# Kernel optimization log

Hardware: AMD Instinct MI355X
Metric: run time of the kernel (lower is better)

The kernel has to match this reference:

```python
import jax, jax.numpy as jnp
import numpy as np
from jax import lax

C = 384        # in_channels
K = 16         # number of frames selected (self.k)
SIGMA = 0.05   # perturbation sigma (forward arg, hardcoded)
NUM_SAMPLES = 500


def setup_inputs() -> dict:
    key = jax.random.key(0)
    ks = jax.random.split(key, 8)
    B, T, N = 16, 32, 196
    D = 2 * C  # PredictorLG embed_dim for 'tpool'
    w = lambda k, s: jax.random.normal(k, s, jnp.float32) * 0.02
    return {
        "x": jax.random.normal(ks[0], (B, T * N, C), jnp.float32),
        "noise": jax.random.normal(ks[1], (B, NUM_SAMPLES, T), jnp.float32),
        "ln_g": jnp.ones((D,), jnp.float32),
        "ln_b": jnp.zeros((D,), jnp.float32),
        "w_in": w(ks[2], (D, D)), "b_in": jnp.zeros((D,), jnp.float32),
        "w1": w(ks[3], (D, D // 2)), "b1": jnp.zeros((D // 2,), jnp.float32),
        "w2": w(ks[4], (D // 2, D // 4)), "b2": jnp.zeros((D // 4,), jnp.float32),
        "w3": w(ks[5], (D // 4, 1)), "b3": jnp.zeros((1,), jnp.float32),
        "N": N, "T": T,
    }


def _predictor(x_, ln_g, ln_b, w_in, b_in, w1, b1, w2, b2, w3, b3):
    # PredictorLG: LayerNorm -> Linear -> GELU -> local/global split -> MLP -> scalar score
    mu = x_.mean(-1, keepdims=True)
    var = x_.var(-1, keepdims=True)  # biased, matches nn.LayerNorm
    h = (x_ - mu) / jnp.sqrt(var + 1e-5) * ln_g + ln_b
    h = jax.nn.gelu(h @ w_in + b_in, approximate=False)
    half = h.shape[-1] // 2
    g = h[..., half:].mean(axis=1, keepdims=True)                      # global pool over T
    h = jnp.concatenate([h[..., :half], jnp.broadcast_to(g, h[..., :half].shape)], -1)
    h = jax.nn.gelu(h @ w1 + b1, approximate=False)
    h = jax.nn.gelu(h @ w2 + b2, approximate=False)
    return (h @ w3 + b3)[..., 0]                                       # (B, T)


def reference(x, noise, ln_g, ln_b, w_in, b_in, w1, b1, w2, b2, w3, b3, N, T):
    B = x.shape[0]
    xt = x.reshape(B, T, N, C)                                         # b t n c
    x_ = jnp.concatenate([xt.mean(2), xt.max(2)], -1)                  # (B, T, 2C)
    scores = _predictor(x_, ln_g, ln_b, w_in, b_in, w1, b1, w2, b2, w3, b3)
    lo = scores.min(-1, keepdims=True)
    hi = scores.max(-1, keepdims=True)
    scores = (scores - lo) / (hi - lo + 1e-5)                          # min_max_norm
    # PerturbedTopKFunction.forward
    perturbed = scores[:, None, :] + noise * SIGMA                     # (B, ns, T)
    idx = jnp.sort(lax.top_k(perturbed, K)[1], axis=-1)                # (B, ns, K)
    indicators = jax.nn.one_hot(idx, T, dtype=x.dtype).mean(1)         # (B, K, T)
    # extract_patches_from_indicators: einsum over flattened frames
    patches = jnp.einsum('bkt,btc->bkc', indicators, xt.reshape(B, T, N * C))
    return patches.reshape(B, K * N, C)                                # 'b k (n c) -> b (k n) c'
```

## Files before the change

kernel.cpp:

```cpp
#include <hip/hip_runtime.h>
#include <math.h>

#define CC 384
#define DD 768
#define TT 32
#define NN 196
#define BB 16
#define KK 16
#define NSAMP 500
#define JV 18816
#define FRAME 75264

__device__ __forceinline__ float gelu_exact(float x) {
    return 0.5f * x * (1.0f + erff(x * 0.70710678118654752440f));
}

__global__ __launch_bounds__(384) void pool_kernel(const float* __restrict__ x,
                                                   const float* __restrict__ ln_g,
                                                   const float* __restrict__ ln_b,
                                                   float* __restrict__ xbar) {
    int row = blockIdx.x;
    const float4* xp = (const float4*)(x + (size_t)row * NN * CC);
    int tx = threadIdx.x;
    int ty = threadIdx.y;
    float4 s = make_float4(0.f, 0.f, 0.f, 0.f);
    float4 m = make_float4(-INFINITY, -INFINITY, -INFINITY, -INFINITY);
    for (int n = ty; n < NN; n += 4) {
        float4 v = xp[n * 96 + tx];
        s.x += v.x; s.y += v.y; s.z += v.z; s.w += v.w;
        m.x = fmaxf(m.x, v.x); m.y = fmaxf(m.y, v.y);
        m.z = fmaxf(m.z, v.z); m.w = fmaxf(m.w, v.w);
    }
    __shared__ float4 ssum[4][96];
    __shared__ float4 smax[4][96];
    __shared__ float xf[DD];
    ssum[ty][tx] = s;
    smax[ty][tx] = m;
    __syncthreads();
    if (ty == 0) {
        for (int r = 1; r < 4; ++r) {
            float4 a = ssum[r][tx];
            s.x += a.x; s.y += a.y; s.z += a.z; s.w += a.w;
            float4 b = smax[r][tx];
            m.x = fmaxf(m.x, b.x); m.y = fmaxf(m.y, b.y);
            m.z = fmaxf(m.z, b.z); m.w = fmaxf(m.w, b.w);
        }
        const float invn = 1.0f / (float)NN;
        xf[4*tx+0] = s.x * invn; xf[4*tx+1] = s.y * invn;
        xf[4*tx+2] = s.z * invn; xf[4*tx+3] = s.w * invn;
        xf[CC + 4*tx+0] = m.x; xf[CC + 4*tx+1] = m.y;
        xf[CC + 4*tx+2] = m.z; xf[CC + 4*tx+3] = m.w;
    }
    __syncthreads();
    int tid = ty * 96 + tx;
    float e0 = xf[tid], e1 = xf[tid + CC];
    float ps = e0 + e1, pq = e0 * e0 + e1 * e1;
    #pragma unroll
    for (int off = 32; off; off >>= 1) {
        ps += __shfl_down(ps, off);
        pq += __shfl_down(pq, off);
    }
    __shared__ float red[12];
    __shared__ float mv[2];
    int wv = tid >> 6;
    if ((tid & 63) == 0) { red[wv] = ps; red[6 + wv] = pq; }
    __syncthreads();
    if (tid == 0) {
        float su = 0.f, sq = 0.f;
        #pragma unroll
        for (int i = 0; i < 6; ++i) { su += red[i]; sq += red[6 + i]; }
        float mean = su * (1.0f / DD);
        float var  = sq * (1.0f / DD) - mean * mean;
        mv[0] = mean;
        mv[1] = rsqrtf(var + 1e-5f);
    }
    __syncthreads();
    float mean = mv[0], inv = mv[1];
    float* o = xbar + (size_t)row * DD;
    o[tid]      = (e0 - mean) * inv * ln_g[tid]      + ln_b[tid];
    o[tid + CC] = (e1 - mean) * inv * ln_g[tid + CC] + ln_b[tid + CC];
}

__global__ __launch_bounds__(256) void fcinA_kernel(const float* __restrict__ xbar,
                                                    const float* __restrict__ w_in,
                                                    float* __restrict__ pfc) {
    __shared__ float xs[8][96];
    int tid = threadIdx.x;
    int row0 = blockIdx.x * 8;
    int col  = blockIdx.y * 256 + tid;
    int k0   = blockIdx.z * 96;
    if (tid < 192) {
        int r = tid / 24, j = tid % 24;
        ((float4*)xs[r])[j] = *(const float4*)(xbar + (size_t)(row0 + r) * DD + k0 + 4 * j);
    }
    __syncthreads();

    float acc[8] = {0.f, 0.f, 0.f, 0.f, 0.f, 0.f, 0.f, 0.f};
    const float* wp = w_in + (size_t)k0 * DD + col;
    #pragma unroll 2
    for (int i = 0; i < 96; i += 4) {
        float w0 = wp[(size_t)(i + 0) * DD];
        float w1 = wp[(size_t)(i + 1) * DD];
        float w2 = wp[(size_t)(i + 2) * DD];
        float w3 = wp[(size_t)(i + 3) * DD];
        #pragma unroll
        for (int r = 0; r < 8; ++r) {
            float4 xv = *(const float4*)&xs[r][i];
            acc[r] += xv.x * w0 + xv.y * w1 + xv.z * w2 + xv.w * w3;
        }
    }
    float* o = pfc + ((size_t)blockIdx.z * 512 + row0) * DD + col;
    #pragma unroll
    for (int r = 0; r < 8; ++r) o[(size_t)r * DD] = acc[r];
}

__global__ __launch_bounds__(256) void fcinB_kernel(const float* __restrict__ pfc,
                                                    const float* __restrict__ b_in,
                                                    float* __restrict__ h1) {
    int gid = blockIdx.x * 256 + threadIdx.x;
    int row = gid / 192, c4 = gid % 192;
    const float4* p4 = (const float4*)pfc;
    float4 s = ((const float4*)b_in)[c4];
    #pragma unroll
    for (int kc = 0; kc < 8; ++kc) {
        float4 v = p4[((size_t)kc * 512 + row) * 192 + c4];
        s.x += v.x; s.y += v.y; s.z += v.z; s.w += v.w;
    }
    float4 r;
    r.x = gelu_exact(s.x); r.y = gelu_exact(s.y);
    r.z = gelu_exact(s.z); r.w = gelu_exact(s.w);
    ((float4*)h1)[(size_t)row * 192 + c4] = r;
}

__global__ __launch_bounds__(128) void gpoolG_kernel(const float* __restrict__ h1,
                                                     const float* __restrict__ w1,
                                                     float* __restrict__ G) {
    __shared__ float gs[CC];
    int tid = threadIdx.x;
    int b = blockIdx.x;
    const float* hb = h1 + (size_t)b * TT * DD + CC;
    for (int i = tid; i < CC; i += 128) {
        float s = 0.f;
        #pragma unroll 8
        for (int t = 0; t < TT; ++t) s += hb[(size_t)t * DD + i];
        gs[i] = s * (1.0f / TT);
    }
    __syncthreads();
    int col = blockIdx.y * 128 + tid;
    float acc = 0.f;
    const float* wp = w1 + (size_t)CC * CC + col;
    #pragma unroll 16
    for (int i = 0; i < CC; ++i)
        acc += gs[i] * wp[(size_t)i * CC];
    G[b * CC + col] = acc;
}

__global__ __launch_bounds__(192) void mlp1A_kernel(const float* __restrict__ h1,
                                                    const float* __restrict__ w1,
                                                    float* __restrict__ pm1) {
    __shared__ float xs[4][96];
    int tid = threadIdx.x;
    int row0 = blockIdx.x * 4;
    int col  = blockIdx.y * 192 + tid;
    int k0   = blockIdx.z * 96;
    if (tid < 96) {
        int r = tid / 24, j = tid % 24;
        ((float4*)xs[r])[j] = *(const float4*)(h1 + (size_t)(row0 + r) * DD + k0 + 4 * j);
    }
    __syncthreads();

    float acc[4] = {0.f, 0.f, 0.f, 0.f};
    const float* wp = w1 + (size_t)k0 * CC + col;
    #pragma unroll 2
    for (int i = 0; i < 96; i += 4) {
        float w0 = wp[(size_t)(i + 0) * CC];
        float w1v = wp[(size_t)(i + 1) * CC];
        float w2 = wp[(size_t)(i + 2) * CC];
        float w3 = wp[(size_t)(i + 3) * CC];
        #pragma unroll
        for (int r = 0; r < 4; ++r) {
            float4 xv = *(const float4*)&xs[r][i];
            acc[r] += xv.x * w0 + xv.y * w1v + xv.z * w2 + xv.w * w3;
        }
    }
    float* o = pm1 + ((size_t)blockIdx.z * 512 + row0) * CC + col;
    #pragma unroll
    for (int r = 0; r < 4; ++r) o[(size_t)r * CC] = acc[r];
}

__global__ __launch_bounds__(256) void mlp1B_kernel(const float* __restrict__ pm1,
                                                    const float* __restrict__ G,
                                                    const float* __restrict__ b1,
                                                    float* __restrict__ h2) {
    int gid = blockIdx.x * 256 + threadIdx.x;
    int row = gid / 96, c4 = gid % 96;
    int b = row >> 5;
    const float4* p4 = (const float4*)pm1;
    float4 s = ((const float4*)b1)[c4];
    float4 gv = ((const float4*)G)[b * 96 + c4];
    s.x += gv.x; s.y += gv.y; s.z += gv.z; s.w += gv.w;
    #pragma unroll
    for (int kc = 0; kc < 4; ++kc) {
        float4 v = p4[((size_t)kc * 512 + row) * 96 + c4];
        s.x += v.x; s.y += v.y; s.z += v.z; s.w += v.w;
    }
    float4 r;
    r.x = gelu_exact(s.x); r.y = gelu_exact(s.y);
    r.z = gelu_exact(s.z); r.w = gelu_exact(s.w);
    ((float4*)h2)[(size_t)row * 96 + c4] = r;
}

__global__ __launch_bounds__(192) void mlp2A_kernel(const float* __restrict__ h2,
                                                    const float* __restrict__ w2,
                                                    float* __restrict__ pm2) {
    __shared__ float xs[192];
    int tid = threadIdx.x;
    int row = blockIdx.x;
    int k0  = blockIdx.y * 192;
    if (tid < 48)
        ((float4*)xs)[tid] = *(const float4*)(h2 + (size_t)row * CC + k0 + 4 * tid);
    __syncthreads();

    float acc = 0.f;
    const float* wp = w2 + (size_t)k0 * 192 + tid;
    #pragma unroll 4
    for (int i = 0; i < 192; i += 4) {
        float w0 = wp[(size_t)(i + 0) * 192];
        float w1 = wp[(size_t)(i + 1) * 192];
        float w2v = wp[(size_t)(i + 2) * 192];
        float w3 = wp[(size_t)(i + 3) * 192];
        float4 xv = *(const float4*)&xs[i];
        acc += xv.x * w0 + xv.y * w1 + xv.z * w2v + xv.w * w3;
    }
    pm2[((size_t)blockIdx.y * 512 + row) * 192 + tid] = acc;
}

__global__ __launch_bounds__(192) void mlp2B_kernel(const float* __restrict__ pm2,
                                                    const float* __restrict__ b2,
                                                    const float* __restrict__ w3,
                                                    const float* __restrict__ b3,
                                                    float* __restrict__ scores) {
    int row = blockIdx.x, tid = threadIdx.x;
    float a = pm2[(size_t)row * 192 + tid]
            + pm2[((size_t)512 + row) * 192 + tid]
            + b2[tid];
    float v = gelu_exact(a) * w3[tid];
    #pragma unroll
    for (int off = 32; off; off >>= 1) v += __shfl_down(v, off);
    __shared__ float red[3];
    if ((tid & 63) == 0) red[tid >> 6] = v;
    __syncthreads();
    if (tid == 0) scores[row] = red[0] + red[1] + red[2] + b3[0];
}

__global__ __launch_bounds__(512) void topk_kernel(const float* __restrict__ scores,
                                                   const float* __restrict__ noise,
                                                   float* __restrict__ ind) {
    __shared__ float ns[TT];
    __shared__ float mnmx[2];
    __shared__ int counts[KK * TT];
    int b = blockIdx.x, tid = threadIdx.x;

    if (tid < TT) ns[tid] = scores[b * TT + tid];
    counts[tid & 511] = 0;
    __syncthreads();
    if (tid == 0) {
        float mn = ns[0], mx = ns[0];
        for (int t = 1; t < TT; ++t) { mn = fminf(mn, ns[t]); mx = fmaxf(mx, ns[t]); }
        mnmx[0] = mn; mnmx[1] = mx;
    }
    __syncthreads();
    if (tid < TT) ns[tid] = (ns[tid] - mnmx[0]) / (mnmx[1] - mnmx[0] + 1e-5f);
    __syncthreads();

    if (tid < NSAMP) {
        const float* nb = noise + ((size_t)b * NSAMP + tid) * TT;
        float p[TT];
        #pragma unroll
        for (int t = 0; t < TT; ++t) p[t] = ns[t] + nb[t] * 0.05f;
        int k = 0;
        #pragma unroll
        for (int t = 0; t < TT; ++t) {
            int rank = 0;
            #pragma unroll
            for (int u = 0; u < TT; ++u)
                rank += (p[u] > p[t] || (p[u] == p[t] && u < t)) ? 1 : 0;
            if (rank < KK) { atomicAdd(&counts[k * TT + t], 1); ++k; }
        }
    }
    __syncthreads();
    ind[b * (KK * TT) + tid] = (float)counts[tid] * (1.0f / NSAMP);
}

__global__ __launch_bounds__(256) void gather_kernel(const float* __restrict__ x,
                                                     const float* __restrict__ ind,
                                                     float* __restrict__ out) {
    __shared__ float w[KK * TT];
    __shared__ int act[TT];
    __shared__ int nact_s;
    int b = blockIdx.y;
    int tid = threadIdx.x;
    w[tid] = ind[b * (KK * TT) + tid];
    w[256 + tid] = ind[b * (KK * TT) + 256 + tid];
    __syncthreads();
    if (tid == 0) {
        int n = 0;
        for (int t = 0; t < TT; ++t) {
            float s = 0.f;
            #pragma unroll
            for (int k = 0; k < KK; ++k) s += w[k * TT + t];
            if (s != 0.f) act[n++] = t;
        }
        nact_s = n;
    }
    __syncthreads();
    int nact = nact_s;

    int j4 = blockIdx.x * 256 + tid;
    if (j4 >= JV) return;

    const float4* xb = (const float4*)(x + (size_t)b * TT * FRAME);
    float4 acc[KK];
    #pragma unroll
    for (int k = 0; k < KK; ++k) acc[k] = make_float4(0.f, 0.f, 0.f, 0.f);

    for (int it = 0; it < nact; ++it) {
        int t = act[it];
        float4 v = xb[(size_t)t * JV + j4];
        #pragma unroll
        for (int k = 0; k < KK; ++k) {
            float wk = w[k * TT + t];
            acc[k].x += wk * v.x; acc[k].y += wk * v.y;
            acc[k].z += wk * v.z; acc[k].w += wk * v.w;
        }
    }
    float4* ob = (float4*)(out + (size_t)b * KK * FRAME);
    #pragma unroll
    for (int k = 0; k < KK; ++k)
        ob[(size_t)k * JV + j4] = acc[k];
}

extern "C" void kernel_launch(void* const* d_in, const int* in_sizes, int n_in,
                              void* d_out, int out_size, void* d_ws, size_t ws_size,
                              hipStream_t stream) {
    const float* x     = (const float*)d_in[0];
    const float* noise = (const float*)d_in[1];
    const float* ln_g  = (const float*)d_in[2];
    const float* ln_b  = (const float*)d_in[3];
    const float* w_in  = (const float*)d_in[4];
    const float* b_in  = (const float*)d_in[5];
    const float* w1    = (const float*)d_in[6];
    const float* b1    = (const float*)d_in[7];
    const float* w2    = (const float*)d_in[8];
    const float* b2    = (const float*)d_in[9];
    const float* w3    = (const float*)d_in[10];
    const float* b3    = (const float*)d_in[11];
    float* out = (float*)d_out;

    float* ws     = (float*)d_ws;
    float* xbar   = ws;
    float* h1     = xbar + 512 * DD;
    float* h2     = h1 + 512 * DD;
    float* scores = h2 + 512 * CC;
    float* ind    = scores + 512;
    float* G      = ind + BB * KK * TT;
    float* pfc    = G + BB * CC;
    float* pm1    = pfc + 8 * 512 * DD;
    float* pm2    = pm1 + 4 * 512 * CC;

    hipLaunchKernelGGL(pool_kernel, dim3(BB * TT), dim3(96, 4), 0, stream,
                       x, ln_g, ln_b, xbar);
    hipLaunchKernelGGL(fcinA_kernel, dim3(64, 3, 8), dim3(256), 0, stream,
                       xbar, w_in, pfc);
    hipLaunchKernelGGL(fcinB_kernel, dim3(384), dim3(256), 0, stream,
                       pfc, b_in, h1);
    hipLaunchKernelGGL(gpoolG_kernel, dim3(BB, 3), dim3(128), 0, stream,
                       h1, w1, G);
    hipLaunchKernelGGL(mlp1A_kernel, dim3(128, 2, 4), dim3(192), 0, stream,
                       h1, w1, pm1);
    hipLaunchKernelGGL(mlp1B_kernel, dim3(192), dim3(256), 0, stream,
                       pm1, G, b1, h2);
    hipLaunchKernelGGL(mlp2A_kernel, dim3(512, 2), dim3(192), 0, stream,
                       h2, w2, pm2);
    hipLaunchKernelGGL(mlp2B_kernel, dim3(512), dim3(192), 0, stream,
                       pm2, b2, w3, b3, scores);
    hipLaunchKernelGGL(topk_kernel, dim3(BB), dim3(512), 0, stream, scores, noise, ind);
    hipLaunchKernelGGL(gather_kernel, dim3((JV + 255) / 256, BB), dim3(256), 0, stream,
                       x, ind, out);
}
```

Measured before the change: 135.7 us.

## Fuse predictor MLP stages into mid kernel and score+topk kernel

Replaces the seven small kernels (fcin reduction, global pool, mlp1 split/reduce, mlp2 split/reduce, topk) with two kernels. One fuses the fcin partial-sum reduction and GELU into the mlp1 matmul and global-pool blocks. The other computes h2, mlp2, the final score and top-k inside one block per batch. This removes intermediate buffers and launch overhead, in exchange for less parallelism in the mlp2 stage (16 blocks) and redundant re-reduction of the fcin partials. The b3 bias is dropped because min-max normalization cancels it.

```diff
diff --git a/kernel.cpp b/kernel.cpp
--- a/kernel.cpp
+++ b/kernel.cpp
@@ -114,163 +114,134 @@
     for (int r = 0; r < 8; ++r) o[(size_t)r * DD] = acc[r];
 }
 
-__global__ __launch_bounds__(256) void fcinB_kernel(const float* __restrict__ pfc,
-                                                    const float* __restrict__ b_in,
-                                                    float* __restrict__ h1) {
-    int gid = blockIdx.x * 256 + threadIdx.x;
-    int row = gid / 192, c4 = gid % 192;
-    const float4* p4 = (const float4*)pfc;
-    float4 s = ((const float4*)b_in)[c4];
-    #pragma unroll
-    for (int kc = 0; kc < 8; ++kc) {
-        float4 v = p4[((size_t)kc * 512 + row) * 192 + c4];
-        s.x += v.x; s.y += v.y; s.z += v.z; s.w += v.w;
-    }
-    float4 r;
-    r.x = gelu_exact(s.x); r.y = gelu_exact(s.y);
-    r.z = gelu_exact(s.z); r.w = gelu_exact(s.w);
-    ((float4*)h1)[(size_t)row * 192 + c4] = r;
-}
-
-__global__ __launch_bounds__(128) void gpoolG_kernel(const float* __restrict__ h1,
-                                                     const float* __restrict__ w1,
-                                                     float* __restrict__ G) {
+__global__ __launch_bounds__(192) void mid_kernel(const float* __restrict__ pfc,
+                                                  const float* __restrict__ b_in,
+                                                  const float* __restrict__ w1,
+                                                  float* __restrict__ pm1,
+                                                  float* __restrict__ G) {
+    __shared__ float xs[4][96];
     __shared__ float gs[CC];
+    int blk = blockIdx.x;
     int tid = threadIdx.x;
-    int b = blockIdx.x;
-    const float* hb = h1 + (size_t)b * TT * DD + CC;
-    for (int i = tid; i < CC; i += 128) {
-        float s = 0.f;
+
+    if (blk < 1024) {
+        int kc = blk & 3, colg = (blk >> 2) & 1, rowg = blk >> 3;
+        int row0 = rowg * 4, col = colg * 192 + tid, k0 = kc * 96;
+        for (int e = tid; e < 384; e += 192) {
+            int r = e / 96, kk = e % 96;
+            int row = row0 + r, k = k0 + kk;
+            float s = b_in[k];
+            #pragma unroll
+            for (int c8 = 0; c8 < 8; ++c8)
+                s += pfc[((size_t)c8 * 512 + row) * DD + k];
+            xs[r][kk] = gelu_exact(s);
+        }
+        __syncthreads();
+
+        float acc[4] = {0.f, 0.f, 0.f, 0.f};
+        const float* wp = w1 + (size_t)k0 * CC + col;
+        #pragma unroll 2
+        for (int i = 0; i < 96; i += 4) {
+            float w0 = wp[(size_t)(i + 0) * CC];
+            float w1v = wp[(size_t)(i + 1) * CC];
+            float w2 = wp[(size_t)(i + 2) * CC];
+            float w3 = wp[(size_t)(i + 3) * CC];
+            #pragma unroll
+            for (int r = 0; r < 4; ++r) {
+                float4 xv = *(const float4*)&xs[r][i];
+                acc[r] += xv.x * w0 + xv.y * w1v + xv.z * w2 + xv.w * w3;
+            }
+        }
+        float* o = pm1 + ((size_t)kc * 512 + row0) * CC + col;
+        #pragma unroll
+        for (int r = 0; r < 4; ++r) o[(size_t)r * CC] = acc[r];
+    } else {
+        int q = blk - 1024;
+        int b = q >> 1, colg = q & 1;
+        for (int i = tid; i < CC; i += 192) {
+            float bias = b_in[CC + i];
+            float s = 0.f;
+            for (int t = 0; t < TT; ++t) {
+                float v = bias;
+                #pragma unroll
+                for (int c8 = 0; c8 < 8; ++c8)
+                    v += pfc[((size_t)c8 * 512 + b * TT + t) * DD + CC + i];
+                s += gelu_exact(v);
+            }
+            gs[i] = s * (1.0f / TT);
+        }
+        __syncthreads();
+        int col = colg * 192 + tid;
+        float acc = 0.f;
+        const float* wp = w1 + (size_t)CC * CC + col;
         #pragma unroll 8
-        for (int t = 0; t < TT; ++t) s += hb[(size_t)t * DD + i];
-        gs[i] = s * (1.0f / TT);
-    }
-    __syncthreads();
-    int col = blockIdx.y * 128 + tid;
-    float acc = 0.f;
-    const float* wp = w1 + (size_t)CC * CC + col;
-    #pragma unroll 16
-    for (int i = 0; i < CC; ++i)
-        acc += gs[i] * wp[(size_t)i * CC];
-    G[b * CC + col] = acc;
-}
-
-__global__ __launch_bounds__(192) void mlp1A_kernel(const float* __restrict__ h1,
-                                                    const float* __restrict__ w1,
-                                                    float* __restrict__ pm1) {
-    __shared__ float xs[4][96];
-    int tid = threadIdx.x;
-    int row0 = blockIdx.x * 4;
-    int col  = blockIdx.y * 192 + tid;
-    int k0   = blockIdx.z * 96;
-    if (tid < 96) {
-        int r = tid / 24, j = tid % 24;
-        ((float4*)xs[r])[j] = *(const float4*)(h1 + (size_t)(row0 + r) * DD + k0 + 4 * j);
-    }
-    __syncthreads();
-
-    float acc[4] = {0.f, 0.f, 0.f, 0.f};
-    const float* wp = w1 + (size_t)k0 * CC + col;
-    #pragma unroll 2
-    for (int i = 0; i < 96; i += 4) {
-        float w0 = wp[(size_t)(i + 0) * CC];
-        float w1v = wp[(size_t)(i + 1) * CC];
-        float w2 = wp[(size_t)(i + 2) * CC];
-        float w3 = wp[(size_t)(i + 3) * CC];
-        #pragma unroll
-        for (int r = 0; r < 4; ++r) {
-            float4 xv = *(const float4*)&xs[r][i];
-            acc[r] += xv.x * w0 + xv.y * w1v + xv.z * w2 + xv.w * w3;
-        }
-    }
-    float* o = pm1 + ((size_t)blockIdx.z * 512 + row0) * CC + col;
-    #pragma unroll
-    for (int r = 0; r < 4; ++r) o[(size_t)r * CC] = acc[r];
-}
-
-__global__ __launch_bounds__(256) void mlp1B_kernel(const float* __restrict__ pm1,
-                                                    const float* __restrict__ G,
-                                                    const float* __restrict__ b1,
-                                                    float* __restrict__ h2) {
-    int gid = blockIdx.x * 256 + threadIdx.x;
-    int row = gid / 96, c4 = gid % 96;
-    int b = row >> 5;
-    const float4* p4 = (const float4*)pm1;
-    float4 s = ((const float4*)b1)[c4];
-    float4 gv = ((const float4*)G)[b * 96 + c4];
-    s.x += gv.x; s.y += gv.y; s.z += gv.z; s.w += gv.w;
-    #pragma unroll
-    for (int kc = 0; kc < 4; ++kc) {
-        float4 v = p4[((size_t)kc * 512 + row) * 96 + c4];
-        s.x += v.x; s.y += v.y; s.z += v.z; s.w += v.w;
-    }
-    float4 r;
-    r.x = gelu_exact(s.x); r.y = gelu_exact(s.y);
-    r.z = gelu_exact(s.z); r.w = gelu_exact(s.w);
-    ((float4*)h2)[(size_t)row * 96 + c4] = r;
-}
-
-__global__ __launch_bounds__(192) void mlp2A_kernel(const float* __restrict__ h2,
-                                                    const float* __restrict__ w2,
-                                                    float* __restrict__ pm2) {
-    __shared__ float xs[192];
-    int tid = threadIdx.x;
-    int row = blockIdx.x;
-    int k0  = blockIdx.y * 192;
-    if (tid < 48)
-        ((float4*)xs)[tid] = *(const float4*)(h2 + (size_t)row * CC + k0 + 4 * tid);
-    __syncthreads();
-
-    float acc = 0.f;
-    const float* wp = w2 + (size_t)k0 * 192 + tid;
-    #pragma unroll 4
-    for (int i = 0; i < 192; i += 4) {
-        float w0 = wp[(size_t)(i + 0) * 192];
-        float w1 = wp[(size_t)(i + 1) * 192];
-        float w2v = wp[(size_t)(i + 2) * 192];
-        float w3 = wp[(size_t)(i + 3) * 192];
-        float4 xv = *(const float4*)&xs[i];
-        acc += xv.x * w0 + xv.y * w1 + xv.z * w2v + xv.w * w3;
-    }
-    pm2[((size_t)blockIdx.y * 512 + row) * 192 + tid] = acc;
-}
-
-__global__ __launch_bounds__(192) void mlp2B_kernel(const float* __restrict__ pm2,
-                                                    const float* __restrict__ b2,
-                                                    const float* __restrict__ w3,
-                                                    const float* __restrict__ b3,
-                                                    float* __restrict__ scores) {
-    int row = blockIdx.x, tid = threadIdx.x;
-    float a = pm2[(size_t)row * 192 + tid]
-            + pm2[((size_t)512 + row) * 192 + tid]
-            + b2[tid];
-    float v = gelu_exact(a) * w3[tid];
-    #pragma unroll
-    for (int off = 32; off; off >>= 1) v += __shfl_down(v, off);
-    __shared__ float red[3];
-    if ((tid & 63) == 0) red[tid >> 6] = v;
-    __syncthreads();
-    if (tid == 0) scores[row] = red[0] + red[1] + red[2] + b3[0];
-}
-
-__global__ __launch_bounds__(512) void topk_kernel(const float* __restrict__ scores,
-                                                   const float* __restrict__ noise,
-                                                   float* __restrict__ ind) {
+        for (int i = 0; i < CC; ++i)
+            acc += gs[i] * wp[(size_t)i * CC];
+        G[b * CC + col] = acc;
+    }
+}
+
+__global__ __launch_bounds__(512) void score_topk_kernel(const float* __restrict__ pm1,
+                                                         const float* __restrict__ G,
+                                                         const float* __restrict__ b1,
+                                                         const float* __restrict__ w2,
+                                                         const float* __restrict__ b2,
+                                                         const float* __restrict__ w3,
+                                                         const float* __restrict__ noise,
+                                                         float* __restrict__ ind) {
+    __shared__ float h2s[32][385];
+    __shared__ float srow[TT];
     __shared__ float ns[TT];
     __shared__ float mnmx[2];
     __shared__ int counts[KK * TT];
     int b = blockIdx.x, tid = threadIdx.x;
 
-    if (tid < TT) ns[tid] = scores[b * TT + tid];
-    counts[tid & 511] = 0;
-    __syncthreads();
+    counts[tid] = 0;
+    for (int e = tid; e < 32 * CC; e += 512) {
+        int r = e / CC, k = e % CC;
+        int row = b * TT + r;
+        float s = b1[k] + G[b * CC + k];
+        #pragma unroll
+        for (int kc = 0; kc < 4; ++kc)
+            s += pm1[((size_t)kc * 512 + row) * CC + k];
+        h2s[r][k] = gelu_exact(s);
+    }
+    __syncthreads();
+
+    {
+        int r = tid >> 4, ch = tid & 15;
+        float acc[12];
+        #pragma unroll
+        for (int j = 0; j < 12; ++j) acc[j] = 0.f;
+        const float4* wq = (const float4*)w2;
+        for (int k = 0; k < CC; ++k) {
+            float hv = h2s[r][k];
+            float4 wa = wq[k * 48 + ch * 3 + 0];
+            float4 wb = wq[k * 48 + ch * 3 + 1];
+            float4 wc = wq[k * 48 + ch * 3 + 2];
+            acc[0] += hv * wa.x; acc[1] += hv * wa.y; acc[2]  += hv * wa.z; acc[3]  += hv * wa.w;
+            acc[4] += hv * wb.x; acc[5] += hv * wb.y; acc[6]  += hv * wb.z; acc[7]  += hv * wb.w;
+            acc[8] += hv * wc.x; acc[9] += hv * wc.y; acc[10] += hv * wc.z; acc[11] += hv * wc.w;
+        }
+        float part = 0.f;
+        #pragma unroll
+        for (int j = 0; j < 12; ++j) {
+            int c = ch * 12 + j;
+            part += gelu_exact(acc[j] + b2[c]) * w3[c];
+        }
+        #pragma unroll
+        for (int off = 8; off; off >>= 1) part += __shfl_down(part, off);
+        if (ch == 0) srow[r] = part;
+    }
+    __syncthreads();
+
     if (tid == 0) {
-        float mn = ns[0], mx = ns[0];
-        for (int t = 1; t < TT; ++t) { mn = fminf(mn, ns[t]); mx = fmaxf(mx, ns[t]); }
+        float mn = srow[0], mx = srow[0];
+        for (int t = 1; t < TT; ++t) { mn = fminf(mn, srow[t]); mx = fmaxf(mx, srow[t]); }
         mnmx[0] = mn; mnmx[1] = mx;
     }
     __syncthreads();
-    if (tid < TT) ns[tid] = (ns[tid] - mnmx[0]) / (mnmx[1] - mnmx[0] + 1e-5f);
+    if (tid < TT) ns[tid] = (srow[tid] - mnmx[0]) / (mnmx[1] - mnmx[0] + 1e-5f);
     __syncthreads();
 
     if (tid < NSAMP) {
@@ -355,36 +326,24 @@
     const float* b2    = (const float*)d_in[9];
     const float* w3    = (const float*)d_in[10];
     const float* b3    = (const float*)d_in[11];
+    (void)b3;
     float* out = (float*)d_out;
 
-    float* ws     = (float*)d_ws;
-    float* xbar   = ws;
-    float* h1     = xbar + 512 * DD;
-    float* h2     = h1 + 512 * DD;
-    float* scores = h2 + 512 * CC;
-    float* ind    = scores + 512;
-    float* G      = ind + BB * KK * TT;
-    float* pfc    = G + BB * CC;
-    float* pm1    = pfc + 8 * 512 * DD;
-    float* pm2    = pm1 + 4 * 512 * CC;
+    float* ws   = (float*)d_ws;
+    float* xbar = ws;
+    float* pfc  = xbar + 512 * DD;
+    float* pm1  = pfc + 8 * 512 * DD;
+    float* G    = pm1 + 4 * 512 * CC;
+    float* ind  = G + BB * CC;
 
     hipLaunchKernelGGL(pool_kernel, dim3(BB * TT), dim3(96, 4), 0, stream,
                        x, ln_g, ln_b, xbar);
     hipLaunchKernelGGL(fcinA_kernel, dim3(64, 3, 8), dim3(256), 0, stream,
                        xbar, w_in, pfc);
-    hipLaunchKernelGGL(fcinB_kernel, dim3(384), dim3(256), 0, stream,
-                       pfc, b_in, h1);
-    hipLaunchKernelGGL(gpoolG_kernel, dim3(BB, 3), dim3(128), 0, stream,
-                       h1, w1, G);
-    hipLaunchKernelGGL(mlp1A_kernel, dim3(128, 2, 4), dim3(192), 0, stream,
-                       h1, w1, pm1);
-    hipLaunchKernelGGL(mlp1B_kernel, dim3(192), dim3(256), 0, stream,
-                       pm1, G, b1, h2);
-    hipLaunchKernelGGL(mlp2A_kernel, dim3(512, 2), dim3(192), 0, stream,
-                       h2, w2, pm2);
-    hipLaunchKernelGGL(mlp2B_kernel, dim3(512), dim3(192), 0, stream,
-                       pm2, b2, w3, b3, scores);
-    hipLaunchKernelGGL(topk_kernel, dim3(BB), dim3(512), 0, stream, scores, noise, ind);
+    hipLaunchKernelGGL(mid_kernel, dim3(1056), dim3(192), 0, stream,
+                       pfc, b_in, w1, pm1, G);
+    hipLaunchKernelGGL(score_topk_kernel, dim3(BB), dim3(512), 0, stream,
+                       pm1, G, b1, w2, b2, w3, noise, ind);
     hipLaunchKernelGGL(gather_kernel, dim3((JV + 255) / 256, BB), dim3(256), 0, stream,
                        x, ind, out);
 }
```

New measurement: 213.6 us. 1.57x slower.
